# Performance work log

Measured on AMD Instinct MI355X. Metric: run time of the kernel, lower is better.

The kernel has to match this reference:

```python
import jax, jax.numpy as jnp
import numpy as np

R = 16
ALPHA = 32
SCALING = ALPHA / R  # 2.0


def setup_inputs() -> dict:
    key = jax.random.key(0)
    k_x, k_w, k_b, k_a, k_bm = jax.random.split(key, 5)
    d = 1024
    x = jax.random.normal(k_x, (4, 4096, d), dtype=jnp.float32)
    W = jax.random.normal(k_w, (d, d), dtype=jnp.float32) * 0.02
    b = jax.random.normal(k_b, (d,), dtype=jnp.float32) * 0.02
    A = jax.random.normal(k_a, (R, d), dtype=jnp.float32) * 0.02
    B = jax.random.normal(k_bm, (d, R), dtype=jnp.float32) * 0.02
    return {"x": x, "W": W, "b": b, "A": A, "B": B}


def reference(x, W, b, A, B):
    # base linear: x @ W^T + b   (W: [out, in])
    base = jnp.einsum("bsd,od->bso", x, W) + b
    # low-rank update: (x @ A^T) @ B^T, scaled (dropout p=0 -> identity)
    u = jnp.einsum("bsd,rd->bsr", x, A)   # [B, S, r]
    update = jnp.einsum("bsr,or->bso", u, B)
    return base + SCALING * update
```

## Files before the change

kernel.cpp:

```cpp
#include <hip/hip_runtime.h>


typedef __bf16 bf16x8 __attribute__((ext_vector_type(8)));
typedef float f32x4 __attribute__((ext_vector_type(4)));
typedef unsigned short ushort8 __attribute__((ext_vector_type(8)));

__device__ __forceinline__ unsigned short f2bf(float f) {
    __bf16 h = (__bf16)f;
    union { __bf16 b; unsigned short u; } v; v.b = h; return v.u;
}
__device__ __forceinline__ ushort8 cvt8u(f32x4 a, f32x4 b) {
    ushort8 o;
#pragma unroll
    for (int i = 0; i < 4; ++i) { o[i] = f2bf(a[i]); o[i + 4] = f2bf(b[i]); }
    return o;
}
__device__ __forceinline__ bf16x8 cvt8(f32x4 a, f32x4 b) {
    union { ushort8 u; bf16x8 h; } v; v.u = cvt8u(a, b); return v.h;
}
__device__ __forceinline__ void gld16(const void* g, void* l) {
    __builtin_amdgcn_global_load_lds(
        (const __attribute__((address_space(1))) unsigned int*)g,
        (__attribute__((address_space(3))) unsigned int*)l, 16, 0, 0);
}

#define FENCE() asm volatile("" ::: "memory")
#define BARRIER() do { FENCE(); __builtin_amdgcn_s_barrier(); FENCE(); } while (0)

__global__ __launch_bounds__(256) void prep(
    const float* __restrict__ W, const float* __restrict__ A,
    const float* __restrict__ B, unsigned short* __restrict__ Weff)
{
    const int idx = blockIdx.x * 256 + threadIdx.x;
    const int o  = idx >> 7;
    const int kc = (idx & 127) << 3;
    float br[16];
#pragma unroll
    for (int r = 0; r < 16; ++r) br[r] = 2.0f * B[o * 16 + r];
    float acc[8];
    const float* wrow = W + (size_t)o * 1024 + kc;
#pragma unroll
    for (int j = 0; j < 8; ++j) acc[j] = wrow[j];
#pragma unroll
    for (int r = 0; r < 16; ++r) {
        const float* arow = A + r * 1024 + kc;
#pragma unroll
        for (int j = 0; j < 8; ++j) acc[j] += br[r] * arow[j];
    }
    ushort8 o8;
#pragma unroll
    for (int j = 0; j < 8; ++j) o8[j] = f2bf(acc[j]);
    *(ushort8*)(Weff + (size_t)o * 1024 + kc) = o8;
}

__global__ __launch_bounds__(512, 4) void gemm256(
    const float* __restrict__ Xf,
    const unsigned short* __restrict__ Wt,
    const float* __restrict__ bias,
    float* __restrict__ out)
{
    extern __shared__ __align__(16) char lds[];

    const int t    = threadIdx.x;
    const int lane = t & 63;
    const int w    = t >> 6;
    const int wr   = w & 3;
    const int wc   = w >> 2;
    const int r16  = lane & 15;
    const int quad = lane >> 4;

    const int nwg = gridDim.x;
    int swz = blockIdx.x;
    if ((nwg & 7) == 0) swz = (swz & 7) * (nwg >> 3) + (swz >> 3);
    const int bm = (swz >> 3) * 256;
    const int bn = (swz & 7) * 128;

    const int ar = t >> 3;
    const int ac = (t & 7) ^ (ar & 7);
    const float* gA = Xf + (size_t)(bm + ar) * 1024 + ac * 4;
    const int adst = t * 16;

    const int brw = t >> 2;
    const int bcc = (t & 3) ^ ((brw >> 1) & 3);
    const unsigned short* pB = Wt + (size_t)(bn + brw) * 1024 + bcc * 8;
    const int bdst = 32768 + t * 16;

    const int o0  = ((2 * quad) ^ (r16 & 7)) * 16;
    const int o1  = ((2 * quad + 1) ^ (r16 & 7)) * 16;
    const int hA0 = (wr * 16 + r16) * 128;
    const int hA1 = ((4 + wr) * 16 + r16) * 128;
    const int bB0 = 32768 + (wc * 16 + r16) * 64 + (quad ^ ((r16 >> 1) & 3)) * 16;

    f32x4 acc[4][4];
#pragma unroll
    for (int i = 0; i < 4; ++i)
#pragma unroll
        for (int jj = 0; jj < 4; ++jj)
            acc[i][jj] = (f32x4){0.f, 0.f, 0.f, 0.f};

#define STAGE_A(HALF, BUF, K)                                                     \
    do { gld16(gA + (HALF) * 131072 + (K),         lds + (BUF) + (HALF) * 16384 + adst);        \
         gld16(gA + (HALF) * 131072 + 65536 + (K), lds + (BUF) + (HALF) * 16384 + 8192 + adst); \
         FENCE(); } while (0)
#define STAGE_B(BUF, K)                                                           \
    do { gld16(pB + (K), lds + (BUF) + bdst); FENCE(); } while (0)

    STAGE_A(0, 0, 0);
    STAGE_B(0, 0);
    STAGE_A(1, 0, 0);
    STAGE_A(0, 40960, 32);
    STAGE_B(40960, 32);
    asm volatile("s_waitcnt vmcnt(3)" ::: "memory");
    BARRIER();

#pragma unroll 2
    for (int j = 0; j < 32; ++j) {
        const int cur = (j & 1) * 40960;
        const int nxt = cur ^ 40960;

        f32x4 a0l = *(const f32x4*)(lds + cur + hA0 + o0);
        f32x4 a0h = *(const f32x4*)(lds + cur + hA0 + o1);
        f32x4 a1l = *(const f32x4*)(lds + cur + hA1 + o0);
        f32x4 a1h = *(const f32x4*)(lds + cur + hA1 + o1);
        bf16x8 fb[4];
#pragma unroll
        for (int nt = 0; nt < 4; ++nt)
            fb[nt] = *(const bf16x8*)(lds + cur + bB0 + nt * 2048);
        if (j < 31) STAGE_A(1, nxt, (j + 1) * 32);
        BARRIER();
        asm volatile("s_waitcnt lgkmcnt(0)" ::: "memory");
        __builtin_amdgcn_sched_barrier(0);
        __builtin_amdgcn_s_setprio(1);
        {
            bf16x8 fa0 = cvt8(a0l, a0h), fa1 = cvt8(a1l, a1h);
#pragma unroll
            for (int nt = 0; nt < 4; ++nt) {
                acc[0][nt] = __builtin_amdgcn_mfma_f32_16x16x32_bf16(fa0, fb[nt], acc[0][nt], 0, 0, 0);
                acc[1][nt] = __builtin_amdgcn_mfma_f32_16x16x32_bf16(fa1, fb[nt], acc[1][nt], 0, 0, 0);
            }
        }
        __builtin_amdgcn_s_setprio(0);
        BARRIER();

        f32x4 a2l = *(const f32x4*)(lds + cur + 16384 + hA0 + o0);
        f32x4 a2h = *(const f32x4*)(lds + cur + 16384 + hA0 + o1);
        f32x4 a3l = *(const f32x4*)(lds + cur + 16384 + hA1 + o0);
        f32x4 a3h = *(const f32x4*)(lds + cur + 16384 + hA1 + o1);
        if (j < 30) { STAGE_A(0, cur, (j + 2) * 32); STAGE_B(cur, (j + 2) * 32); }
        if (j < 30)       asm volatile("s_waitcnt vmcnt(3)" ::: "memory");
        else if (j == 30) asm volatile("s_waitcnt vmcnt(0)" ::: "memory");
        BARRIER();
        asm volatile("s_waitcnt lgkmcnt(0)" ::: "memory");
        __builtin_amdgcn_sched_barrier(0);
        __builtin_amdgcn_s_setprio(1);
        {
            bf16x8 fa2 = cvt8(a2l, a2h), fa3 = cvt8(a3l, a3h);
#pragma unroll
            for (int nt = 0; nt < 4; ++nt) {
                acc[2][nt] = __builtin_amdgcn_mfma_f32_16x16x32_bf16(fa2, fb[nt], acc[2][nt], 0, 0, 0);
                acc[3][nt] = __builtin_amdgcn_mfma_f32_16x16x32_bf16(fa3, fb[nt], acc[3][nt], 0, 0, 0);
            }
        }
        __builtin_amdgcn_s_setprio(0);
        BARRIER();
    }
#undef STAGE_A
#undef STAGE_B

    const int orow0 = bm + wr * 16 + quad * 4;
    const int ocol0 = bn + wc * 16 + r16;
#pragma unroll
    for (int nt = 0; nt < 4; ++nt) {
        const float bv = bias[ocol0 + nt * 32];
#pragma unroll
        for (int mt = 0; mt < 4; ++mt) {
            float* orow = out + (size_t)(orow0 + mt * 64) * 1024 + (ocol0 + nt * 32);
#pragma unroll
            for (int i = 0; i < 4; ++i)
                orow[(size_t)i * 1024] = acc[mt][nt][i] + bv;
        }
    }
}

template <bool XF32>
__global__ __launch_bounds__(256) void gemm_bt(
    const void* __restrict__ X_, const unsigned short* __restrict__ Wt,
    const float* __restrict__ bias, float* __restrict__ out)
{
    __shared__ __align__(16) unsigned short lA[128 * 32];
    __shared__ __align__(16) unsigned short lB[128 * 32];

    const int t    = threadIdx.x;
    const int lane = t & 63;
    const int w    = t >> 6;
    const int bm   = blockIdx.x * 128;
    const int bn   = blockIdx.y * 128;
    const int wm   = (w & 1) * 64;
    const int wn   = (w >> 1) * 64;
    const int r16  = lane & 15;
    const int quad = lane >> 4;

    const int srow = t >> 2;
    const int gc   = (t & 3) ^ ((srow >> 1) & 3);
    unsigned short* lsA = lA + t * 8;
    unsigned short* lsB = lB + t * 8;
    const size_t ga0 = (size_t)(bm + srow) * 1024 + gc * 8;
    const size_t ga1 = (size_t)(bm + srow + 64) * 1024 + gc * 8;
    const unsigned short* gB0 = Wt + (size_t)(bn + srow) * 1024 + gc * 8;

    const int p    = (quad ^ ((r16 >> 1) & 3)) * 8;
    const int aoff = (wm + r16) * 32 + p;
    const int boff = (wn + r16) * 32 + p;

    const unsigned short* Xb = (const unsigned short*)X_;
    const float*          Xf = (const float*)X_;

    f32x4 acc[4][4];
#pragma unroll
    for (int i = 0; i < 4; ++i)
#pragma unroll
        for (int j = 0; j < 4; ++j) {
            f32x4 z = {0.f, 0.f, 0.f, 0.f};
            acc[i][j] = z;
        }

    for (int kt = 0; kt < 1024; kt += 32) {
        if (XF32) {
            f32x4 a0 = *(const f32x4*)(Xf + ga0 + kt);
            f32x4 a1 = *(const f32x4*)(Xf + ga0 + kt + 4);
            f32x4 a2 = *(const f32x4*)(Xf + ga1 + kt);
            f32x4 a3 = *(const f32x4*)(Xf + ga1 + kt + 4);
            *(ushort8*)lsA          = cvt8u(a0, a1);
            *(ushort8*)(lsA + 2048) = cvt8u(a2, a3);
        } else {
            gld16(Xb + ga0 + kt, lsA);
            gld16(Xb + ga1 + kt, lsA + 2048);
        }
        gld16(gB0 + kt,             lsB);
        gld16(gB0 + kt + 64 * 1024, lsB + 2048);
        __syncthreads();

        bf16x8 fa[4], fb[4];
#pragma unroll
        for (int mt = 0; mt < 4; ++mt) fa[mt] = *(const bf16x8*)(lA + aoff + mt * 16 * 32);
#pragma unroll
        for (int nt = 0; nt < 4; ++nt) fb[nt] = *(const bf16x8*)(lB + boff + nt * 16 * 32);

#pragma unroll
        for (int mt = 0; mt < 4; ++mt)
#pragma unroll
            for (int nt = 0; nt < 4; ++nt)
                acc[mt][nt] = __builtin_amdgcn_mfma_f32_16x16x32_bf16(
                    fa[mt], fb[nt], acc[mt][nt], 0, 0, 0);

        __syncthreads();
    }

    const int orow0 = bm + wm + quad * 4;
    const int ocol0 = bn + wn + r16;
#pragma unroll
    for (int nt = 0; nt < 4; ++nt) {
        const float bv = bias[ocol0 + nt * 16];
#pragma unroll
        for (int mt = 0; mt < 4; ++mt)
#pragma unroll
            for (int i = 0; i < 4; ++i)
                out[(size_t)(orow0 + mt * 16 + i) * 1024 + (ocol0 + nt * 16)] =
                    acc[mt][nt][i] + bv;
    }
}

extern "C" void kernel_launch(void* const* d_in, const int* in_sizes, int n_in,
                              void* d_out, int out_size, void* d_ws, size_t ws_size,
                              hipStream_t stream) {
    const float* x  = (const float*)d_in[0];
    const float* W  = (const float*)d_in[1];
    const float* b  = (const float*)d_in[2];
    const float* A  = (const float*)d_in[3];
    const float* Bm = (const float*)d_in[4];
    float* out = (float*)d_out;

    const int M = in_sizes[0] / 1024;

    const bool fast = (ws_size >= (2u << 20) + 4096) && (M % 256 == 0);
    unsigned short* Weff = (unsigned short*)d_ws;
    hipLaunchKernelGGL(prep, dim3(512), dim3(256), 0, stream, W, A, Bm, Weff);
    if (fast) {
        hipLaunchKernelGGL(gemm256, dim3((M / 256) * 8), dim3(512), 81920, stream,
                           x, Weff, b, out);
    } else {
        hipLaunchKernelGGL((gemm_bt<true>), dim3(M / 128, 8), dim3(256), 0, stream,
                           (const void*)x, Weff, b, out);
    }
}
```

Baseline: 178.9 us.

## Reshape GEMM block tile from 256x128 to 128x256 with split B staging

Changes the main GEMM work-group tile from 256 rows by 128 columns to 128 rows by 256 columns, so each block stages one 128-row fp32 X tile and two halves of the bf16 weight tile per K step. The f32-to-bf16 conversion of A fragments now happens once per K step and is reused across both column halves, and LDS use drops from 80 KB to 64 KB per block. The intent is to cut the fp32 activation traffic and conversion work per output element, since X is the larger fp32 operand. The cost is more reloading of the bf16 weight tile and a different grid shape and swizzle.

```diff
diff --git a/kernel.cpp b/kernel.cpp
--- a/kernel.cpp
+++ b/kernel.cpp
@@ -72,8 +72,8 @@
     const int nwg = gridDim.x;
     int swz = blockIdx.x;
     if ((nwg & 7) == 0) swz = (swz & 7) * (nwg >> 3) + (swz >> 3);
-    const int bm = (swz >> 3) * 256;
-    const int bn = (swz & 7) * 128;
+    const int bm = (swz >> 2) * 128;
+    const int bn = (swz & 3) * 256;
 
     const int ar = t >> 3;
     const int ac = (t & 7) ^ (ar & 7);
@@ -82,41 +82,42 @@
 
     const int brw = t >> 2;
     const int bcc = (t & 3) ^ ((brw >> 1) & 3);
-    const unsigned short* pB = Wt + (size_t)(bn + brw) * 1024 + bcc * 8;
-    const int bdst = 32768 + t * 16;
-
-    const int o0  = ((2 * quad) ^ (r16 & 7)) * 16;
-    const int o1  = ((2 * quad + 1) ^ (r16 & 7)) * 16;
-    const int hA0 = (wr * 16 + r16) * 128;
-    const int hA1 = ((4 + wr) * 16 + r16) * 128;
-    const int bB0 = 32768 + (wc * 16 + r16) * 64 + (quad ^ ((r16 >> 1) & 3)) * 16;
-
-    f32x4 acc[4][4];
-#pragma unroll
-    for (int i = 0; i < 4; ++i)
-#pragma unroll
-        for (int jj = 0; jj < 4; ++jj)
+    const unsigned short* pB0 = Wt + (size_t)(bn + brw) * 1024 + bcc * 8;
+    const unsigned short* pB1 = pB0 + 131072;
+    const int bdst = t * 16;
+
+    const int o0 = ((2 * quad) ^ (r16 & 7)) * 16;
+    const int o1 = ((2 * quad + 1) ^ (r16 & 7)) * 16;
+    const int hA0 = ((wr * 2 + 0) * 16 + r16) * 128;
+    const int hA1 = ((wr * 2 + 1) * 16 + r16) * 128;
+    const int bB0 = 16384 + (wc * 16 + r16) * 64 + (quad ^ ((r16 >> 1) & 3)) * 16;
+
+    f32x4 acc[2][8];
+#pragma unroll
+    for (int i = 0; i < 2; ++i)
+#pragma unroll
+        for (int jj = 0; jj < 8; ++jj)
             acc[i][jj] = (f32x4){0.f, 0.f, 0.f, 0.f};
 
-#define STAGE_A(HALF, BUF, K)                                                     \
-    do { gld16(gA + (HALF) * 131072 + (K),         lds + (BUF) + (HALF) * 16384 + adst);        \
-         gld16(gA + (HALF) * 131072 + 65536 + (K), lds + (BUF) + (HALF) * 16384 + 8192 + adst); \
+#define STAGE_A(BUF, K)                                                        \
+    do { gld16(gA + (K),             lds + (BUF) + adst);                      \
+         gld16(gA + 65536 + (K),     lds + (BUF) + 8192 + adst);               \
          FENCE(); } while (0)
-#define STAGE_B(BUF, K)                                                           \
-    do { gld16(pB + (K), lds + (BUF) + bdst); FENCE(); } while (0)
-
-    STAGE_A(0, 0, 0);
-    STAGE_B(0, 0);
-    STAGE_A(1, 0, 0);
-    STAGE_A(0, 40960, 32);
-    STAGE_B(40960, 32);
+#define STAGE_B0(BUF, K) do { gld16(pB0 + (K), lds + (BUF) + 16384 + bdst); FENCE(); } while (0)
+#define STAGE_B1(BUF, K) do { gld16(pB1 + (K), lds + (BUF) + 24576 + bdst); FENCE(); } while (0)
+
+    STAGE_A(0, 0);
+    STAGE_B0(0, 0);
+    STAGE_B1(0, 0);
+    STAGE_A(32768, 32);
+    STAGE_B0(32768, 32);
     asm volatile("s_waitcnt vmcnt(3)" ::: "memory");
     BARRIER();
 
 #pragma unroll 2
     for (int j = 0; j < 32; ++j) {
-        const int cur = (j & 1) * 40960;
-        const int nxt = cur ^ 40960;
+        const int cur = (j & 1) * 32768;
+        const int nxt = cur ^ 32768;
 
         f32x4 a0l = *(const f32x4*)(lds + cur + hA0 + o0);
         f32x4 a0h = *(const f32x4*)(lds + cur + hA0 + o1);
@@ -126,55 +127,50 @@
 #pragma unroll
         for (int nt = 0; nt < 4; ++nt)
             fb[nt] = *(const bf16x8*)(lds + cur + bB0 + nt * 2048);
-        if (j < 31) STAGE_A(1, nxt, (j + 1) * 32);
+        if (j < 31) STAGE_B1(nxt, (j + 1) * 32);
         BARRIER();
         asm volatile("s_waitcnt lgkmcnt(0)" ::: "memory");
         __builtin_amdgcn_sched_barrier(0);
         __builtin_amdgcn_s_setprio(1);
-        {
-            bf16x8 fa0 = cvt8(a0l, a0h), fa1 = cvt8(a1l, a1h);
-#pragma unroll
-            for (int nt = 0; nt < 4; ++nt) {
-                acc[0][nt] = __builtin_amdgcn_mfma_f32_16x16x32_bf16(fa0, fb[nt], acc[0][nt], 0, 0, 0);
-                acc[1][nt] = __builtin_amdgcn_mfma_f32_16x16x32_bf16(fa1, fb[nt], acc[1][nt], 0, 0, 0);
-            }
+        bf16x8 fa0 = cvt8(a0l, a0h), fa1 = cvt8(a1l, a1h);
+#pragma unroll
+        for (int nt = 0; nt < 4; ++nt) {
+            acc[0][nt] = __builtin_amdgcn_mfma_f32_16x16x32_bf16(fa0, fb[nt], acc[0][nt], 0, 0, 0);
+            acc[1][nt] = __builtin_amdgcn_mfma_f32_16x16x32_bf16(fa1, fb[nt], acc[1][nt], 0, 0, 0);
         }
         __builtin_amdgcn_s_setprio(0);
         BARRIER();
 
-        f32x4 a2l = *(const f32x4*)(lds + cur + 16384 + hA0 + o0);
-        f32x4 a2h = *(const f32x4*)(lds + cur + 16384 + hA0 + o1);
-        f32x4 a3l = *(const f32x4*)(lds + cur + 16384 + hA1 + o0);
-        f32x4 a3h = *(const f32x4*)(lds + cur + 16384 + hA1 + o1);
-        if (j < 30) { STAGE_A(0, cur, (j + 2) * 32); STAGE_B(cur, (j + 2) * 32); }
+#pragma unroll
+        for (int nt = 0; nt < 4; ++nt)
+            fb[nt] = *(const bf16x8*)(lds + cur + bB0 + 8192 + nt * 2048);
+        if (j < 30) { STAGE_A(cur, (j + 2) * 32); STAGE_B0(cur, (j + 2) * 32); }
         if (j < 30)       asm volatile("s_waitcnt vmcnt(3)" ::: "memory");
         else if (j == 30) asm volatile("s_waitcnt vmcnt(0)" ::: "memory");
         BARRIER();
         asm volatile("s_waitcnt lgkmcnt(0)" ::: "memory");
         __builtin_amdgcn_sched_barrier(0);
         __builtin_amdgcn_s_setprio(1);
-        {
-            bf16x8 fa2 = cvt8(a2l, a2h), fa3 = cvt8(a3l, a3h);
-#pragma unroll
-            for (int nt = 0; nt < 4; ++nt) {
-                acc[2][nt] = __builtin_amdgcn_mfma_f32_16x16x32_bf16(fa2, fb[nt], acc[2][nt], 0, 0, 0);
-                acc[3][nt] = __builtin_amdgcn_mfma_f32_16x16x32_bf16(fa3, fb[nt], acc[3][nt], 0, 0, 0);
-            }
+#pragma unroll
+        for (int nt = 0; nt < 4; ++nt) {
+            acc[0][nt + 4] = __builtin_amdgcn_mfma_f32_16x16x32_bf16(fa0, fb[nt], acc[0][nt + 4], 0, 0, 0);
+            acc[1][nt + 4] = __builtin_amdgcn_mfma_f32_16x16x32_bf16(fa1, fb[nt], acc[1][nt + 4], 0, 0, 0);
         }
         __builtin_amdgcn_s_setprio(0);
         BARRIER();
     }
 #undef STAGE_A
-#undef STAGE_B
-
-    const int orow0 = bm + wr * 16 + quad * 4;
+#undef STAGE_B0
+#undef STAGE_B1
+
+    const int orow0 = bm + wr * 32 + quad * 4;
     const int ocol0 = bn + wc * 16 + r16;
 #pragma unroll
-    for (int nt = 0; nt < 4; ++nt) {
+    for (int nt = 0; nt < 8; ++nt) {
         const float bv = bias[ocol0 + nt * 32];
 #pragma unroll
-        for (int mt = 0; mt < 4; ++mt) {
-            float* orow = out + (size_t)(orow0 + mt * 64) * 1024 + (ocol0 + nt * 32);
+        for (int mt = 0; mt < 2; ++mt) {
+            float* orow = out + (size_t)(orow0 + mt * 16) * 1024 + (ocol0 + nt * 32);
 #pragma unroll
             for (int i = 0; i < 4; ++i)
                 orow[(size_t)i * 1024] = acc[mt][nt][i] + bv;
@@ -282,11 +278,11 @@
 
     const int M = in_sizes[0] / 1024;
 
-    const bool fast = (ws_size >= (2u << 20) + 4096) && (M % 256 == 0);
+    const bool fast = (ws_size >= (2u << 20) + 4096) && (M % 128 == 0);
     unsigned short* Weff = (unsigned short*)d_ws;
     hipLaunchKernelGGL(prep, dim3(512), dim3(256), 0, stream, W, A, Bm, Weff);
     if (fast) {
-        hipLaunchKernelGGL(gemm256, dim3((M / 256) * 8), dim3(512), 81920, stream,
+        hipLaunchKernelGGL(gemm256, dim3((M / 128) * 4), dim3(512), 65536, stream,
                            x, Weff, b, out);
     } else {
         hipLaunchKernelGGL((gemm_bt<true>), dim3(M / 128, 8), dim3(256), 0, stream,
```

After: 168.8 us. 1.06x faster.
